# Kernel tuning notes

Hardware: AMD Instinct MI355X
Metric: run time of the kernel (lower is better)

## Reference

```python
import jax, jax.numpy as jnp
import numpy as np

N, C, H, W = 8, 80, 200, 200
PRE_NMS_THRESH = 0.05
PRE_NMS_TOP_N = 1000
NMS_THRESH = 0.6
FPN_POST_NMS_TOP_N = 100
MIN_SIZE = 0.0
TO_REMOVE = 1.0
CLASS_OFFSET = 100000.0  # > any coordinate; separates classes for class-aware NMS


def setup_inputs() -> dict:
    key = jax.random.key(0)
    k1, k2, k3, k4, k5 = jax.random.split(key, 5)
    # logits shifted so sigmoid probs sit near the 0.05 threshold (realistic sparsity)
    box_cls = jax.random.normal(k1, (N, C, H, W), jnp.float32) - 3.0
    box_regression = jax.random.uniform(k2, (N, 4, H, W), jnp.float32) * 64.0
    centerness = jax.random.normal(k3, (N, 1, H, W), jnp.float32)
    locations = jax.random.uniform(k4, (H * W, 2), jnp.float32) * 1600.0
    image_sizes = jax.random.randint(k5, (N, 2), 800, 1600, jnp.int32)  # (h, w)
    return {"locations": locations, "box_cls": box_cls,
            "box_regression": box_regression, "centerness": centerness,
            "image_sizes": image_sizes}


def _pairwise_iou(boxes):
    x1, y1, x2, y2 = boxes[:, 0], boxes[:, 1], boxes[:, 2], boxes[:, 3]
    area = (x2 - x1 + TO_REMOVE) * (y2 - y1 + TO_REMOVE)  # [K]
    iw = jnp.clip(jnp.minimum(x2[:, None], x2[None, :]) - jnp.maximum(x1[:, None], x1[None, :]) + TO_REMOVE, 0.0)
    ih = jnp.clip(jnp.minimum(y2[:, None], y2[None, :]) - jnp.maximum(y1[:, None], y1[None, :]) + TO_REMOVE, 0.0)
    inter = iw * ih
    return inter / (area[:, None] + area[None, :] - inter)


def reference(locations, box_cls, box_regression, centerness, image_sizes):
    n, c, h, w = box_cls.shape
    # [N,C,H,W] -> [N,HW,C] probs; [N,4,H,W] -> [N,HW,4]; centerness -> [N,HW]
    cls_prob = jax.nn.sigmoid(box_cls.transpose(0, 2, 3, 1).reshape(n, -1, c))
    reg = box_regression.transpose(0, 2, 3, 1).reshape(n, -1, 4)
    cent = jax.nn.sigmoid(centerness.transpose(0, 2, 3, 1).reshape(n, -1))

    def per_image(p, r, ct, hw):
        # candidate mask on raw class probs (before centerness weighting), as in source
        cand = p > PRE_NMS_THRESH                      # [HW, C]
        scores = p * ct[:, None]                       # [HW, C]
        flat = jnp.where(cand, scores, -jnp.inf).reshape(-1)
        top_s, top_i = jax.lax.top_k(flat, PRE_NMS_TOP_N)   # sorted desc
        loc_idx = top_i // c
        labels = top_i % c + 1
        valid = top_s > 0.0
        l2 = locations[loc_idx]                        # [K, 2]
        rr = r[loc_idx]                                # [K, 4]
        boxes = jnp.concatenate([l2 - rr[:, :2], l2 + rr[:, 2:]], axis=-1)
        ih = hw[0].astype(jnp.float32)
        iw = hw[1].astype(jnp.float32)
        boxes = jnp.stack([jnp.clip(boxes[:, 0], 0.0, iw - 1.0),
                           jnp.clip(boxes[:, 1], 0.0, ih - 1.0),
                           jnp.clip(boxes[:, 2], 0.0, iw - 1.0),
                           jnp.clip(boxes[:, 3], 0.0, ih - 1.0)], axis=-1)
        bw = boxes[:, 2] - boxes[:, 0] + TO_REMOVE
        bh = boxes[:, 3] - boxes[:, 1] + TO_REMOVE
        valid = valid & (bw >= MIN_SIZE) & (bh >= MIN_SIZE)
        # class-aware NMS via per-class coordinate offset
        ob = boxes + labels.astype(jnp.float32)[:, None] * CLASS_OFFSET
        iou = _pairwise_iou(ob)                        # [K, K]
        K = PRE_NMS_TOP_N
        idxs = jnp.arange(K)
        def body(supp, i):
            keep_i = valid[i] & jnp.logical_not(supp[i])
            supp = supp | (keep_i & (iou[i] > NMS_THRESH) & (idxs != i))
            return supp, keep_i
        _, keep = jax.lax.scan(body, jnp.zeros(K, dtype=bool), idxs)
        fscores = jnp.where(keep & valid, top_s, -jnp.inf)
        fs, fi = jax.lax.top_k(fscores, FPN_POST_NMS_TOP_N)
        fv = fs > 0.0
        fb = boxes[fi] * fv[:, None].astype(boxes.dtype)
        fl = jnp.where(fv, labels[fi], 0).astype(jnp.float32)
        out_s = jnp.where(fv, jnp.sqrt(jnp.where(fv, fs, 1.0)), 0.0)  # sqrt of cls*centerness
        # [K_post, 6] = x1,y1,x2,y2,score,label
        return jnp.concatenate([fb, out_s[:, None], fl[:, None]], axis=-1)

    return jax.vmap(per_image)(cls_prob, reg, cent, image_sizes)
```

## Files before the change

kernel.cpp:

```cpp
#include <hip/hip_runtime.h>
#include <math.h>

#define NIMG 8
#define NCLS 80
#define HW 40000
#define M (NCLS*HW)
#define UBINS 4096
#define CANDL 4096
#define SPILL_CAP 65536
#define BCAP 1024
#define TOPK 1000
#define OUTK 100
#define PRE_T 0.05f
#define NMS_T 0.6f
#define FLOOR_BITS 0x3E800000u
#define FLOOR_SAFE 0.2494f

__device__ unsigned int       g_scnt[NIMG][32];
__device__ unsigned int       g_ovf[NIMG];
__device__ unsigned int       g_hist[NIMG][UBINS];
__device__ unsigned short     g_xthr_b[NIMG * HW];
__device__ float              g_sct[NIMG * HW];
__device__ unsigned long long g_key[NIMG][SPILL_CAP];

__device__ __forceinline__ float sigmoid_exact(float x){
    return 1.0f / (1.0f + expf(-x));
}

__device__ __forceinline__ unsigned long long shfl_xor_u64(unsigned long long v, int j){
    int lo = __shfl_xor((int)(unsigned int)(v & 0xffffffffull), j);
    int hi = __shfl_xor((int)(unsigned int)(v >> 32), j);
    return ((unsigned long long)(unsigned int)hi << 32) | (unsigned long long)(unsigned int)lo;
}

__global__ void k0_init(const float* __restrict__ cent){
    int t = blockIdx.x * blockDim.x + threadIdx.x;
    if (t < NIMG * 32) ((unsigned int*)g_scnt)[t] = 0u;
    if (t < NIMG) g_ovf[t] = 0u;
    if (t < NIMG * UBINS) ((unsigned int*)g_hist)[t] = 0u;
    if (t < NIMG * HW){
        float pct = sigmoid_exact(cent[t]);
        g_sct[t] = pct;
        float a = FLOOR_SAFE / pct;
        float xt;
        if (a >= 1.0f) xt = 3.0e38f;
        else {
            float am = fminf(a, 0.98f);
            xt = logf(am / (1.0f - am));
        }
        unsigned xb = __float_as_uint(xt);
        unsigned hb = xb >> 16;
        if ((xb & 0x80000000u) && (xb & 0xFFFFu)) hb += 1u;
        g_xthr_b[t] = (unsigned short)hb;
    }
}

__global__ void __launch_bounds__(512, 8) k1_spill(const float* __restrict__ cls){
    const int n   = blockIdx.y;
    const int tid = threadIdx.x;
    const int e16 = blockIdx.x * 8192 + tid * 16;
    __shared__ unsigned long long skey[BCAP];
    __shared__ unsigned int lcnt, lbase;
    if (tid == 0) lcnt = 0u;
    __syncthreads();

    if (e16 < M){
        const int c   = e16 / HW;
        const int hw0 = e16 - c * HW;
        const float* pc = cls + (size_t)n * M + e16;
        const unsigned short* pt = g_xthr_b + n * HW + hw0;
        float4 xa[4];
        uint4  tb[2];
        #pragma unroll
        for (int i = 0; i < 4; ++i) xa[i] = *(const float4*)(pc + i * 4);
        tb[0] = *(const uint4*)(pt);
        tb[1] = *(const uint4*)(pt + 8);
        float th[16];
        #pragma unroll
        for (int q = 0; q < 2; ++q){
            unsigned w0 = (q?tb[1].x:tb[0].x), w1 = (q?tb[1].y:tb[0].y);
            unsigned w2 = (q?tb[1].z:tb[0].z), w3 = (q?tb[1].w:tb[0].w);
            th[q*8+0] = __uint_as_float((w0 & 0xFFFFu) << 16);
            th[q*8+1] = __uint_as_float((w0 >> 16) << 16);
            th[q*8+2] = __uint_as_float((w1 & 0xFFFFu) << 16);
            th[q*8+3] = __uint_as_float((w1 >> 16) << 16);
            th[q*8+4] = __uint_as_float((w2 & 0xFFFFu) << 16);
            th[q*8+5] = __uint_as_float((w2 >> 16) << 16);
            th[q*8+6] = __uint_as_float((w3 & 0xFFFFu) << 16);
            th[q*8+7] = __uint_as_float((w3 >> 16) << 16);
        }
        #define SPILL1(HWI, XV, THV) \
        if (XV >= THV){ \
            float p_ = sigmoid_exact(XV); \
            if (p_ > PRE_T){ \
                float s_ = p_ * g_sct[n * HW + (HWI)]; \
                unsigned long long key_ = ((unsigned long long)__float_as_uint(s_) << 32) \
                    | (unsigned long long)(0xFFFFFFFFu - (unsigned int)((HWI) * NCLS + c)); \
                atomicAdd(&g_hist[n][(int)(s_ * 4096.0f)], 1u); \
                unsigned int pp_ = atomicAdd(&lcnt, 1u); \
                if (pp_ < BCAP) skey[pp_] = key_; \
            } \
        }
        #pragma unroll
        for (int i = 0; i < 4; ++i){
            SPILL1(hw0 + i*4 + 0, xa[i].x, th[i*4+0])
            SPILL1(hw0 + i*4 + 1, xa[i].y, th[i*4+1])
            SPILL1(hw0 + i*4 + 2, xa[i].z, th[i*4+2])
            SPILL1(hw0 + i*4 + 3, xa[i].w, th[i*4+3])
        }
        #undef SPILL1
    }

    __syncthreads();
    unsigned int raw = lcnt;
    unsigned int cnt = raw < BCAP ? raw : BCAP;
    if (tid == 0){
        lbase = cnt ? atomicAdd(&g_scnt[n][0], cnt) : 0u;
        if (raw > BCAP) g_ovf[n] = 1u;
    }
    __syncthreads();
    unsigned int base = lbase;
    for (unsigned int i = tid; i < cnt; i += 512){
        unsigned int pos = base + i;
        if (pos < SPILL_CAP) g_key[n][pos] = skey[i];
    }
}

struct SelPhase {
    unsigned int hist[UBINS];
    unsigned int cs[256];
    unsigned int wtot[4];
    unsigned long long keysL[CANDL];
};
struct NmsPhase {
    float ox1[TOPK], oy1[TOPK], ox2[TOPK], oy2[TOPK], oar[TOPK];
    float bxs[TOPK][4];
    float sc[TOPK];
    int   lab[TOPK];
    int   keeplist[OUTK];
    unsigned int  Wc[16][80];
    unsigned int  ctot[80];
    unsigned int  coff[81];
    unsigned int  wcnt[16];
    unsigned short ord[1024];
    unsigned char validf[TOPK];
    unsigned char supp[TOPK];
    unsigned char keepf[1024];
};
union KU { SelPhase sel; NmsPhase nms; };

#define REGSTEP(K_, J_) { \
    unsigned long long pa = shfl_xor_u64(va, (J_)); \
    unsigned long long pb = shfl_xor_u64(vb, (J_)); \
    bool fa = ((tid & (J_)) == 0); \
    bool da = ((tid & (K_)) == 0); \
    bool db = (((tid + 1024) & (K_)) == 0); \
    va = (fa == da) ? (va > pa ? va : pa) : (va < pa ? va : pa); \
    vb = (fa == db) ? (vb > pb ? vb : pb) : (vb < pb ? vb : pb); \
}
#define REGSTEP1(K_, J_) { \
    unsigned long long pa = shfl_xor_u64(va, (J_)); \
    bool fa = ((tid & (J_)) == 0); \
    bool da = ((tid & (K_)) == 0); \
    va = (fa == da) ? (va > pa ? va : pa) : (va < pa ? va : pa); \
}

__global__ void __launch_bounds__(1024) k2_select_nms(const float* __restrict__ cls,
                                                      const float* __restrict__ loc,
                                                      const float* __restrict__ reg,
                                                      const int*   __restrict__ imsz,
                                                      float* __restrict__ out){
    const int n = blockIdx.x;
    const int tid = threadIdx.x;
    const int lane = tid & 63;
    const int wv   = tid >> 6;
    __shared__ KU u;
    __shared__ unsigned long long stop[TOPK];
    __shared__ unsigned int lcnt, s_cut, s_flag, s_nmsfb, s_cnt, s_c, s_csn, s_Cest, s_srtbad;

    for (int i = tid; i < UBINS; i += 1024) u.sel.hist[i] = g_hist[n][i];
    if (tid == 0){ s_nmsfb = 0u; s_srtbad = 0u; s_c = 0xFFFFFFFFu; s_csn = 0u;
                   s_Cest = 0u; s_cut = 0u; lcnt = 0u; }
    if (tid < TOPK) stop[tid] = 0ull;
    __syncthreads();

    unsigned int scnt_raw = g_scnt[n][0];
    unsigned int ovf_f    = g_ovf[n];
    unsigned int S = scnt_raw < SPILL_CAP ? scnt_raw : SPILL_CAP;

    if (tid < 256){
        unsigned int s = 0;
        int base = tid * 16;
        #pragma unroll
        for (int i = 0; i < 16; ++i) s += u.sel.hist[base + i];
        u.sel.cs[tid] = s;
    }
    __syncthreads();
    if (tid < 256){
        unsigned int v = u.sel.cs[tid];
        #pragma unroll
        for (int d = 1; d < 64; d <<= 1){
            unsigned int t = __shfl_down(v, d);
            if (lane + d < 64) v += t;
        }
        if (lane == 0) u.sel.wtot[wv] = v;
        u.sel.cs[tid] = v;
    }
    __syncthreads();
    if (tid < 256){
        unsigned int tail = 0;
        for (int w = wv + 1; w < 4; ++w) tail += u.sel.wtot[w];
        u.sel.cs[tid] += tail;
    }
    __syncthreads();
    if (tid < 256){
        unsigned int a = u.sel.cs[tid];
        unsigned int b = (tid == 255) ? 0u : u.sel.cs[tid + 1];
        if (a >= TOPK && b < TOPK){ s_c = (unsigned int)tid; s_csn = b; }
    }
    __syncthreads();
    if (wv == 0 && s_c != 0xFFFFFFFFu){
        unsigned int cst = s_c;
        unsigned int h = (lane < 16) ? u.sel.hist[cst * 16 + lane] : 0u;
        #pragma unroll
        for (int d = 1; d < 16; d <<= 1){
            unsigned int t = __shfl_down(h, d);
            if (lane + d < 16) h += t;
        }
        unsigned int gs  = h + s_csn;
        unsigned int gsn = __shfl_down(gs, 1);
        if (lane == 15) gsn = s_csn;
        if (lane < 16 && gs >= TOPK && gsn < TOPK){ s_cut = cst * 16 + lane; s_Cest = gs; }
    }
    __syncthreads();
    if (tid == 0){
        unsigned int c025 = u.sel.cs[64];
        s_flag = (scnt_raw > SPILL_CAP) || ovf_f || (s_c == 0xFFFFFFFFu) ||
                 (c025 < TOPK) || (s_Cest > CANDL) ? 1u : 0u;
    }
    __syncthreads();

    if (s_flag){
        for (int i = tid; i < UBINS; i += 1024) u.sel.hist[i] = 0u;
        __syncthreads();
        const float* cls_n = cls + (size_t)n * M;
        const float* sct_n = g_sct + n * HW;
        for (int e = tid; e < M; e += 1024){
            float p = sigmoid_exact(cls_n[e]);
            if (p > PRE_T){
                int c = e / HW; int hw = e - c * HW;
                float s = p * sct_n[hw];
                atomicAdd(&u.sel.hist[(int)(s * 4096.0f)], 1u);
            }
        }
        __syncthreads();
        if (tid < 256){
            unsigned int s = 0;
            int base = tid * 16;
            #pragma unroll
            for (int i = 0; i < 16; ++i) s += u.sel.hist[base + i];
            u.sel.cs[tid] = s;
        }
        __syncthreads();
        if (tid == 0){
            unsigned int acc = 0; int cut = 0; int c = 255;
            for (; c >= 0; --c){ if (acc + u.sel.cs[c] >= TOPK) break; acc += u.sel.cs[c]; }
            if (c >= 0){
                int b = c*16 + 15;
                for (;; --b){ acc += u.sel.hist[b]; if (acc >= TOPK || b == c*16) break; }
                cut = b;
            }
            while (acc > CANDL && cut < UBINS){ acc -= u.sel.hist[cut]; cut++; }
            s_cut = (unsigned int)cut;
        }
        __syncthreads();
        unsigned int cutb = s_cut;
        for (int e = tid; e < M; e += 1024){
            float p = sigmoid_exact(cls_n[e]);
            if (p > PRE_T){
                int c = e / HW; int hw = e - c * HW;
                float s = p * sct_n[hw];
                if ((int)(s * 4096.0f) >= (int)cutb){
                    unsigned int pos = atomicAdd(&lcnt, 1u);
                    if (pos < CANDL){
                        unsigned int idx = (unsigned int)(hw * NCLS + c);
                        u.sel.keysL[pos] = ((unsigned long long)__float_as_uint(s) << 32)
                                         | (unsigned long long)(0xFFFFFFFFu - idx);
                    }
                }
            }
        }
    } else {
        unsigned int cutb = s_cut;
        for (unsigned int i = tid; i < S; i += 1024){
            unsigned long long k = g_key[n][i];
            float s = __uint_as_float((unsigned int)(k >> 32));
            bool pass = ((unsigned int)(int)(s * 4096.0f)) >= cutb;
            unsigned long long mb = __ballot(pass);
            unsigned int wcnt_ = (unsigned int)__popcll(mb);
            unsigned int base = 0;
            if (lane == 0 && wcnt_) base = atomicAdd(&lcnt, wcnt_);
            base = (unsigned int)__builtin_amdgcn_readfirstlane((int)base);
            if (pass){
                unsigned int p = base + (unsigned int)__popcll(mb & ((1ull << lane) - 1ull));
                if (p < CANDL) u.sel.keysL[p] = k;
            }
        }
    }
    __syncthreads();

    int C = (int)(lcnt < CANDL ? lcnt : CANDL);
    unsigned long long kk = 0ull;
    if (C <= 1024){
        for (int i = C + tid; i < 1024; i += 1024) u.sel.keysL[i] = 0ull;
        __syncthreads();
        unsigned long long va = u.sel.keysL[tid];
        REGSTEP1(2,1)
        REGSTEP1(4,2)  REGSTEP1(4,1)
        REGSTEP1(8,4)  REGSTEP1(8,2)  REGSTEP1(8,1)
        REGSTEP1(16,8) REGSTEP1(16,4) REGSTEP1(16,2) REGSTEP1(16,1)
        REGSTEP1(32,16) REGSTEP1(32,8) REGSTEP1(32,4) REGSTEP1(32,2) REGSTEP1(32,1)
        REGSTEP1(64,32) REGSTEP1(64,16) REGSTEP1(64,8) REGSTEP1(64,4) REGSTEP1(64,2) REGSTEP1(64,1)
        for (int k = 128; k <= 1024; k <<= 1){
            u.sel.keysL[tid] = va;
            __syncthreads();
            for (int j = k >> 1; j >= 64; j >>= 1){
                if (tid < 512){
                    int i  = ((tid & ~(j - 1)) << 1) | (tid & (j - 1));
                    int p2 = i | j;
                    unsigned long long a = u.sel.keysL[i];
                    unsigned long long b = u.sel.keysL[p2];
                    bool up = ((i & k) == 0);
                    if (up ? (a < b) : (a > b)){ u.sel.keysL[i] = b; u.sel.keysL[p2] = a; }
                }
                __syncthreads();
            }
            va = u.sel.keysL[tid];
            REGSTEP1(k,32) REGSTEP1(k,16) REGSTEP1(k,8) REGSTEP1(k,4) REGSTEP1(k,2) REGSTEP1(k,1)
        }
        u.sel.keysL[tid] = va;
        __syncthreads();
        if (tid <= 1022 && u.sel.keysL[tid] < u.sel.keysL[tid + 1]) atomicOr(&s_srtbad, 1u);
        __syncthreads();
    } else if (C <= 2048){
        for (int i = C + tid; i < 2048; i += 1024) u.sel.keysL[i] = 0ull;
        __syncthreads();
        unsigned long long va = u.sel.keysL[tid];
        unsigned long long vb = u.sel.keysL[tid + 1024];
        REGSTEP(2,1)
        REGSTEP(4,2)  REGSTEP(4,1)
        REGSTEP(8,4)  REGSTEP(8,2)  REGSTEP(8,1)
        REGSTEP(16,8) REGSTEP(16,4) REGSTEP(16,2) REGSTEP(16,1)
        REGSTEP(32,16) REGSTEP(32,8) REGSTEP(32,4) REGSTEP(32,2) REGSTEP(32,1)
        REGSTEP(64,32) REGSTEP(64,16) REGSTEP(64,8) REGSTEP(64,4) REGSTEP(64,2) REGSTEP(64,1)
        for (int k = 128; k <= 2048; k <<= 1){
            if (k == 2048){
                unsigned long long mx = va > vb ? va : vb;
                unsigned long long mn = va > vb ? vb : va;
                va = mx; vb = mn;
            }
            u.sel.keysL[tid] = va; u.sel.keysL[tid + 1024] = vb;
            __syncthreads();
            for (int j = (k == 2048) ? 512 : (k >> 1); j >= 64; j >>= 1){
                int i  = ((tid & ~(j - 1)) << 1) | (tid & (j - 1));
                int p2 = i | j;
                unsigned long long a = u.sel.keysL[i];
                unsigned long long b = u.sel.keysL[p2];
                bool up = ((i & k) == 0);
                if (up ? (a < b) : (a > b)){ u.sel.keysL[i] = b; u.sel.keysL[p2] = a; }
                __syncthreads();
            }
            va = u.sel.keysL[tid]; vb = u.sel.keysL[tid + 1024];
            REGSTEP(k,32) REGSTEP(k,16) REGSTEP(k,8) REGSTEP(k,4) REGSTEP(k,2) REGSTEP(k,1)
        }
        u.sel.keysL[tid] = va; u.sel.keysL[tid + 1024] = vb;
        __syncthreads();
        bool bad = (u.sel.keysL[tid] < u.sel.keysL[tid + 1]);
        if (tid <= 1022) bad = bad || (u.sel.keysL[tid + 1024] < u.sel.keysL[tid + 1025]);
        if (bad) atomicOr(&s_srtbad, 1u);
        __syncthreads();
    } else {
        for (int i = tid; i < C; i += 1024){
            unsigned long long k = u.sel.keysL[i];
            int rank = 0;
            for (int j = 0; j < C; ++j) rank += (u.sel.keysL[j] > k) ? 1 : 0;
            if (rank < TOPK) stop[rank] = k;
        }
        __syncthreads();
        if (tid < TOPK) u.sel.keysL[tid] = stop[tid];
        __syncthreads();
    }

    if (s_srtbad){
        if (tid == 0) lcnt = 0u;
        __syncthreads();
        unsigned int cutb = s_cut;
        if (s_flag){
            const float* cls_n = cls + (size_t)n * M;
            const float* sct_n = g_sct + n * HW;
            for (int e = tid; e < M; e += 1024){
                float p = sigmoid_exact(cls_n[e]);
                if (p > PRE_T){
                    int c = e / HW; int hw = e - c * HW;
                    float s = p * sct_n[hw];
                    if ((int)(s * 4096.0f) >= (int)cutb){
                        unsigned int pos = atomicAdd(&lcnt, 1u);
                        if (pos < CANDL){
                            unsigned int idx = (unsigned int)(hw * NCLS + c);
                            u.sel.keysL[pos] = ((unsigned long long)__float_as_uint(s) << 32)
                                             | (unsigned long long)(0xFFFFFFFFu - idx);
                        }
                    }
                }
            }
        } else {
            for (unsigned int i = tid; i < S; i += 1024){
                unsigned long long k = g_key[n][i];
                float s = __uint_as_float((unsigned int)(k >> 32));
                bool pass = ((unsigned int)(int)(s * 4096.0f)) >= cutb;
                unsigned long long mb = __ballot(pass);
                unsigned int wcnt_ = (unsigned int)__popcll(mb);
                unsigned int base = 0;
                if (lane == 0 && wcnt_) base = atomicAdd(&lcnt, wcnt_);
                base = (unsigned int)__builtin_amdgcn_readfirstlane((int)base);
                if (pass){
                    unsigned int p = base + (unsigned int)__popcll(mb & ((1ull << lane) - 1ull));
                    if (p < CANDL) u.sel.keysL[p] = k;
                }
            }
        }
        __syncthreads();
        int C2 = (int)(lcnt < CANDL ? lcnt : CANDL);
        for (int i = C2 + tid; i < 2048; i += 1024) u.sel.keysL[i] = 0ull;
        __syncthreads();
        for (int k = 2; k <= 2048; k <<= 1){
            for (int j = k >> 1; j > 0; j >>= 1){
                int i  = ((tid & ~(j - 1)) << 1) | (tid & (j - 1));
                int p2 = i | j;
                unsigned long long a = u.sel.keysL[i];
                unsigned long long b = u.sel.keysL[p2];
                bool up = ((i & k) == 0);
                if (up ? (a < b) : (a > b)){ u.sel.keysL[i] = b; u.sel.keysL[p2] = a; }
                __syncthreads();
            }
        }
    }
    kk = (tid < TOPK) ? u.sel.keysL[tid] : 0ull;
    __syncthreads();

    float rx1 = 0.f, ry1 = 0.f, rx2 = -1.f, ry2 = -1.f, rar = 1.f;
    float ihh = (float)imsz[2*n + 0];
    float iww = (float)imsz[2*n + 1];

    u.nms.keepf[tid] = 0;
    { unsigned int* wz = &u.nms.Wc[0][0];
      for (int i = tid; i < 16*80; i += 1024) wz[i] = 0u; }

    if (tid < TOPK){
        unsigned int bits = (unsigned int)(kk >> 32);
        float s = __uint_as_float(bits);
        u.nms.supp[tid] = 0;
        if (s > 0.0f){
            unsigned int idx = 0xFFFFFFFFu - (unsigned int)(kk & 0xFFFFFFFFull);
            int hw = (int)(idx / NCLS);
            int c  = (int)(idx % NCLS);
            int l  = c + 1;
            float x  = loc[2*hw], y = loc[2*hw + 1];
            float r0 = reg[((size_t)n*4 + 0)*HW + hw];
            float r1 = reg[((size_t)n*4 + 1)*HW + hw];
            float r2 = reg[((size_t)n*4 + 2)*HW + hw];
            float r3 = reg[((size_t)n*4 + 3)*HW + hw];
            float x1 = fminf(fmaxf(x - r0, 0.0f), iww - 1.0f);
            float y1 = fminf(fmaxf(y - r1, 0.0f), ihh - 1.0f);
            float x2 = fminf(fmaxf(x + r2, 0.0f), iww - 1.0f);
            float y2 = fminf(fmaxf(y + r3, 0.0f), ihh - 1.0f);
            u.nms.bxs[tid][0] = x1; u.nms.bxs[tid][1] = y1;
            u.nms.bxs[tid][2] = x2; u.nms.bxs[tid][3] = y2;
            float off = (float)l * 100000.0f;
            float a1 = x1 + off, b1 = y1 + off, a2 = x2 + off, b2 = y2 + off;
            float ar = (a2 - a1 + 1.0f) * (b2 - b1 + 1.0f);
            u.nms.ox1[tid] = a1; u.nms.oy1[tid] = b1;
            u.nms.ox2[tid] = a2; u.nms.oy2[tid] = b2; u.nms.oar[tid] = ar;
            rx1 = a1; ry1 = b1; rx2 = a2; ry2 = b2; rar = ar;
            u.nms.sc[tid] = s; u.nms.lab[tid] = l; u.nms.validf[tid] = 1;
        } else {
            u.nms.validf[tid] = 0; u.nms.sc[tid] = 0.0f; u.nms.lab[tid] = 0;
            u.nms.bxs[tid][0] = u.nms.bxs[tid][1] = 0.0f;
            u.nms.bxs[tid][2] = u.nms.bxs[tid][3] = 0.0f;
            u.nms.ox1[tid] = 0.f; u.nms.oy1[tid] = 0.f;
            u.nms.ox2[tid] = -1.f; u.nms.oy2[tid] = -1.f; u.nms.oar[tid] = 1.f;
        }
    }
    __syncthreads();

    int mk = -1;
    if (tid < TOPK && u.nms.validf[tid]) mk = u.nms.lab[tid] - 1;
    if (mk >= 0) atomicAdd(&u.nms.Wc[wv][mk], 1u);
    __syncthreads();
    if (tid < NCLS){
        unsigned int acc = 0;
        for (int w = 0; w < 16; ++w){
            unsigned int v = u.nms.Wc[w][tid];
            u.nms.Wc[w][tid] = acc;
            acc += v;
        }
        u.nms.ctot[tid] = acc;
        if (acc > 64) atomicOr(&s_nmsfb, 1u);
    }
    __syncthreads();
    if (wv == 0){
        unsigned int v = u.nms.ctot[lane];
        unsigned int inc = v;
        #pragma unroll
        for (int d = 1; d < 64; d <<= 1){
            unsigned int t = __shfl_up(inc, d);
            if (lane >= d) inc += t;
        }
        u.nms.coff[lane + 1] = inc;
        if (lane == 0) u.nms.coff[0] = 0u;
        unsigned int base = __shfl(inc, 63);
        unsigned int inc2 = (lane < 16) ? u.nms.ctot[64 + lane] : 0u;
        #pragma unroll
        for (int d = 1; d < 16; d <<= 1){
            unsigned int t = __shfl_up(inc2, d);
            if (lane >= d) inc2 += t;
        }
        if (lane < 16) u.nms.coff[65 + lane] = base + inc2;
    }
    __syncthreads();

    if (!s_nmsfb){
        int below = 0;
        for (int l = 0; l < 64; ++l){
            int ok = __shfl(mk, l);
            below += (l < lane && ok == mk) ? 1 : 0;
        }
        if (mk >= 0){
            unsigned int pos = u.nms.coff[mk] + u.nms.Wc[wv][mk] + (unsigned int)below;
            u.nms.ord[pos] = (unsigned short)tid;
        }
        __syncthreads();

        for (int k = wv; k < NCLS; k += 16){
            int base = (int)u.nms.coff[k];
            int ck   = (int)u.nms.coff[k + 1] - base;
            if (ck <= 0) continue;
            int rr = (lane < ck) ? (int)u.nms.ord[base + lane] : -1;
            float bx1 = 0.f, by1 = 0.f, bx2 = -1.f, by2 = -1.f, bar = 1.f;
            if (rr >= 0){
                bx1 = u.nms.ox1[rr]; by1 = u.nms.oy1[rr];
                bx2 = u.nms.ox2[rr]; by2 = u.nms.oy2[rr]; bar = u.nms.oar[rr];
            }
            int sup = 0;
            for (int p = 0; p < ck; ++p){
                int keep_p = !__shfl(sup, p);
                if (keep_p){
                    float px1 = __shfl(bx1, p), py1 = __shfl(by1, p);
                    float px2 = __shfl(bx2, p), py2 = __shfl(by2, p);
                    float par = __shfl(bar, p);
                    if (lane > p && rr >= 0){
                        float ix1 = fmaxf(px1, bx1);
                        float iy1 = fmaxf(py1, by1);
                        float ix2 = fminf(px2, bx2);
                        float iy2 = fminf(py2, by2);
                        float iw_ = fmaxf(ix2 - ix1 + 1.0f, 0.0f);
                        float ih_ = fmaxf(iy2 - iy1 + 1.0f, 0.0f);
                        float inter = iw_ * ih_;
                        float iou = inter / (par + bar - inter);
                        if (iou > NMS_T) sup = 1;
                    }
                }
            }
            if (rr >= 0) u.nms.keepf[rr] = sup ? 0 : 1;
        }
        __syncthreads();

        int kf = (int)u.nms.keepf[tid];
        unsigned long long mb = __ballot(kf != 0);
        if (lane == 0) u.nms.wcnt[wv] = (unsigned int)__popcll(mb);
        __syncthreads();
        if (wv == 0){
            unsigned int v = (lane < 16) ? u.nms.wcnt[lane] : 0u;
            unsigned int orig = v;
            for (int d = 1; d < 16; d <<= 1){
                unsigned int t = __shfl_up(v, d);
                if (lane >= d) v += t;
            }
            if (lane < 16) u.nms.wcnt[lane] = v - orig;
            if (lane == 15) s_cnt = (v < OUTK ? v : OUTK);
        }
        __syncthreads();
        if (kf){
            unsigned int slot = u.nms.wcnt[wv] + (unsigned int)__popcll(mb & ((1ull << lane) - 1ull));
            if (slot < OUTK) u.nms.keeplist[slot] = tid;
        }
    } else {
        int cnt = 0;
        for (int i = 0; i < TOPK; ++i){
            bool keep_i = u.nms.validf[i] && !u.nms.supp[i];
            if (keep_i){
                if (tid == 0) u.nms.keeplist[cnt] = i;
                if (tid < TOPK && tid != i){
                    float ix1 = fmaxf(u.nms.ox1[i], rx1);
                    float iy1 = fmaxf(u.nms.oy1[i], ry1);
                    float ix2 = fminf(u.nms.ox2[i], rx2);
                    float iy2 = fminf(u.nms.oy2[i], ry2);
                    float iw_ = fmaxf(ix2 - ix1 + 1.0f, 0.0f);
                    float ih_ = fmaxf(iy2 - iy1 + 1.0f, 0.0f);
                    float inter = iw_ * ih_;
                    float iou = inter / (u.nms.oar[i] + rar - inter);
                    if (iou > NMS_T) u.nms.supp[tid] = 1;
                }
                cnt++;
                __syncthreads();
                if (cnt == OUTK) break;
            }
        }
        if (tid == 0) s_cnt = (unsigned int)(cnt < OUTK ? cnt : OUTK);
    }
    __syncthreads();

    int cnt = (int)s_cnt;
    if (tid < OUTK){
        float r0=0.f,r1=0.f,r2=0.f,r3=0.f,r4=0.f,r5=0.f;
        if (tid < cnt){
            int i = u.nms.keeplist[tid];
            r0 = u.nms.bxs[i][0]; r1 = u.nms.bxs[i][1];
            r2 = u.nms.bxs[i][2]; r3 = u.nms.bxs[i][3];
            r4 = sqrtf(u.nms.sc[i]); r5 = (float)u.nms.lab[i];
        }
        float* o = out + ((size_t)n*OUTK + tid)*6;
        o[0]=r0; o[1]=r1; o[2]=r2; o[3]=r3; o[4]=r4; o[5]=r5;
    }
}

extern "C" void kernel_launch(void* const* d_in, const int* in_sizes, int n_in,
                              void* d_out, int out_size, void* d_ws, size_t ws_size,
                              hipStream_t stream){
    const float* loc  = (const float*)d_in[0];
    const float* cls  = (const float*)d_in[1];
    const float* reg  = (const float*)d_in[2];
    const float* cent = (const float*)d_in[3];
    const int*   imsz = (const int*)d_in[4];
    float* out = (float*)d_out;

    hipLaunchKernelGGL(k0_init,       dim3(625),                 dim3(512),  0, stream, cent);
    hipLaunchKernelGGL(k1_spill,      dim3((M+8191)/8192, NIMG), dim3(512),  0, stream, cls);
    hipLaunchKernelGGL(k2_select_nms, dim3(NIMG),                dim3(1024), 0, stream,
                       cls, loc, reg, imsz, out);
}
```

Baseline: 238.7 us.

## Split select-and-NMS kernel into cut, parallel collect, sort and NMS kernels

The single per-image select+NMS kernel is split into four launches: a cut-bin computation, a collect step spread over 8 blocks per image that compacts spilled keys above the cut into a global candidate buffer, a register/shared bitonic sort that writes the top-1000 keys to global memory, and the NMS kernel that reads them. The aim is to parallelise the serial scan over the spill buffer, which previously ran on only 8 blocks, and to shrink the NMS kernel's shared-memory footprint. The cost is three extra kernel launches and global-memory round trips, plus a global atomic counter for candidate compaction. The fallback path (flag set) now re-runs the full-scan path inside the NMS kernel.

After: 240.1 us. Within noise of the previous version (+0.6%).

```diff
diff --git a/kernel.cpp b/kernel.cpp
--- a/kernel.cpp
+++ b/kernel.cpp
@@ -22,6 +22,11 @@
 __device__ unsigned short     g_xthr_b[NIMG * HW];
 __device__ float              g_sct[NIMG * HW];
 __device__ unsigned long long g_key[NIMG][SPILL_CAP];
+__device__ unsigned int       g_cut[NIMG];
+__device__ unsigned int       g_flag[NIMG];
+__device__ unsigned int       g_ccnt[NIMG][32];
+__device__ unsigned long long g_cand[NIMG][CANDL];
+__device__ unsigned long long g_top[NIMG][TOPK];
 
 __device__ __forceinline__ float sigmoid_exact(float x){
     return 1.0f / (1.0f + expf(-x));
@@ -36,6 +41,7 @@
 __global__ void k0_init(const float* __restrict__ cent){
     int t = blockIdx.x * blockDim.x + threadIdx.x;
     if (t < NIMG * 32) ((unsigned int*)g_scnt)[t] = 0u;
+    if (t < NIMG * 32) ((unsigned int*)g_ccnt)[t] = 0u;
     if (t < NIMG) g_ovf[t] = 0u;
     if (t < NIMG * UBINS) ((unsigned int*)g_hist)[t] = 0u;
     if (t < NIMG * HW){
@@ -126,10 +132,212 @@
     }
 }
 
+
+__global__ void __launch_bounds__(1024) k2a_cut(){
+    const int n = blockIdx.x;
+    const int tid = threadIdx.x;
+    const int lane = tid & 63;
+    const int wv   = tid >> 6;
+    __shared__ unsigned int hist[UBINS];
+    __shared__ unsigned int cs[256];
+    __shared__ unsigned int wtot[4];
+    __shared__ unsigned int s_c, s_csn, s_cut, s_Cest;
+
+    for (int i = tid; i < UBINS; i += 1024) hist[i] = g_hist[n][i];
+    if (tid == 0){ s_c = 0xFFFFFFFFu; s_csn = 0u; s_cut = 0u; s_Cest = 0u; }
+    __syncthreads();
+
+    unsigned int scnt_raw = g_scnt[n][0];
+    unsigned int ovf_f    = g_ovf[n];
+
+    if (tid < 256){
+        unsigned int s = 0;
+        int base = tid * 16;
+        #pragma unroll
+        for (int i = 0; i < 16; ++i) s += hist[base + i];
+        cs[tid] = s;
+    }
+    __syncthreads();
+    if (tid < 256){
+        unsigned int v = cs[tid];
+        #pragma unroll
+        for (int d = 1; d < 64; d <<= 1){
+            unsigned int t = __shfl_down(v, d);
+            if (lane + d < 64) v += t;
+        }
+        if (lane == 0) wtot[wv] = v;
+        cs[tid] = v;
+    }
+    __syncthreads();
+    if (tid < 256){
+        unsigned int tail = 0;
+        for (int w = wv + 1; w < 4; ++w) tail += wtot[w];
+        cs[tid] += tail;
+    }
+    __syncthreads();
+    if (tid < 256){
+        unsigned int a = cs[tid];
+        unsigned int b = (tid == 255) ? 0u : cs[tid + 1];
+        if (a >= TOPK && b < TOPK){ s_c = (unsigned int)tid; s_csn = b; }
+    }
+    __syncthreads();
+    if (wv == 0 && s_c != 0xFFFFFFFFu){
+        unsigned int cst = s_c;
+        unsigned int h = (lane < 16) ? hist[cst * 16 + lane] : 0u;
+        #pragma unroll
+        for (int d = 1; d < 16; d <<= 1){
+            unsigned int t = __shfl_down(h, d);
+            if (lane + d < 16) h += t;
+        }
+        unsigned int gs  = h + s_csn;
+        unsigned int gsn = __shfl_down(gs, 1);
+        if (lane == 15) gsn = s_csn;
+        if (lane < 16 && gs >= TOPK && gsn < TOPK){ s_cut = cst * 16 + lane; s_Cest = gs; }
+    }
+    __syncthreads();
+    if (tid == 0){
+        unsigned int c025 = cs[64];
+        unsigned int fl = (scnt_raw > SPILL_CAP) || ovf_f || (s_c == 0xFFFFFFFFu) ||
+                          (c025 < TOPK) || (s_Cest > 2048u) ? 1u : 0u;
+        g_cut[n]  = s_cut;
+        g_flag[n] = fl;
+    }
+}
+
+__global__ void __launch_bounds__(1024) k2b_collect(){
+    const int slice = blockIdx.x;
+    const int n     = blockIdx.y;
+    const int tid   = threadIdx.x;
+    const int lane  = tid & 63;
+    if (g_flag[n]) return;
+    unsigned int scnt_raw = g_scnt[n][0];
+    unsigned int S = scnt_raw < SPILL_CAP ? scnt_raw : SPILL_CAP;
+    unsigned int chunk = (S + 7) / 8;
+    unsigned int lo = slice * chunk;
+    unsigned int hi = lo + chunk; if (hi > S) hi = S;
+    unsigned int cutb = g_cut[n];
+    for (unsigned int i = lo + tid; i < hi; i += 1024){
+        unsigned long long k = g_key[n][i];
+        float s = __uint_as_float((unsigned int)(k >> 32));
+        bool pass = ((unsigned int)(int)(s * 4096.0f)) >= cutb;
+        unsigned long long mb = __ballot(pass);
+        unsigned int wcnt_ = (unsigned int)__popcll(mb);
+        unsigned int base = 0;
+        if (lane == 0 && wcnt_) base = atomicAdd(&g_ccnt[n][0], wcnt_);
+        base = (unsigned int)__builtin_amdgcn_readfirstlane((int)base);
+        if (pass){
+            unsigned int p = base + (unsigned int)__popcll(mb & ((1ull << lane) - 1ull));
+            if (p < CANDL) g_cand[n][p] = k;
+        }
+    }
+}
+
+#define REGSTEP(K_, J_) { \
+    unsigned long long pa = shfl_xor_u64(va, (J_)); \
+    unsigned long long pb = shfl_xor_u64(vb, (J_)); \
+    bool fa = ((tid & (J_)) == 0); \
+    bool da = ((tid & (K_)) == 0); \
+    bool db = (((tid + 1024) & (K_)) == 0); \
+    va = (fa == da) ? (va > pa ? va : pa) : (va < pa ? va : pa); \
+    vb = (fa == db) ? (vb > pb ? vb : pb) : (vb < pb ? vb : pb); \
+}
+#define REGSTEP1(K_, J_) { \
+    unsigned long long pa = shfl_xor_u64(va, (J_)); \
+    bool fa = ((tid & (J_)) == 0); \
+    bool da = ((tid & (K_)) == 0); \
+    va = (fa == da) ? (va > pa ? va : pa) : (va < pa ? va : pa); \
+}
+
+__global__ void __launch_bounds__(1024) k2c_sort(){
+    const int n = blockIdx.x;
+    const int tid = threadIdx.x;
+    __shared__ unsigned long long keysL[2048];
+    __shared__ unsigned int s_srtbad;
+    if (g_flag[n]) return;
+    if (tid == 0) s_srtbad = 0u;
+    int C = (int)g_ccnt[n][0];
+    if (C > 2048){ if (tid == 0) atomicOr(&g_flag[n], 2u); return; }
+    for (int i = tid; i < C; i += 1024) if (i < C) keysL[i] = g_cand[n][i];
+    __syncthreads();
+
+    if (C <= 1024){
+        for (int i = C + tid; i < 1024; i += 1024) keysL[i] = 0ull;
+        __syncthreads();
+        unsigned long long va = keysL[tid & 1023];
+        if (tid < 1024){
+            REGSTEP1(2,1)
+            REGSTEP1(4,2)  REGSTEP1(4,1)
+            REGSTEP1(8,4)  REGSTEP1(8,2)  REGSTEP1(8,1)
+            REGSTEP1(16,8) REGSTEP1(16,4) REGSTEP1(16,2) REGSTEP1(16,1)
+            REGSTEP1(32,16) REGSTEP1(32,8) REGSTEP1(32,4) REGSTEP1(32,2) REGSTEP1(32,1)
+            REGSTEP1(64,32) REGSTEP1(64,16) REGSTEP1(64,8) REGSTEP1(64,4) REGSTEP1(64,2) REGSTEP1(64,1)
+        }
+        for (int k = 128; k <= 1024; k <<= 1){
+            keysL[tid] = va;
+            __syncthreads();
+            for (int j = k >> 1; j >= 64; j >>= 1){
+                if (tid < 512){
+                    int i  = ((tid & ~(j - 1)) << 1) | (tid & (j - 1));
+                    int p2 = i | j;
+                    unsigned long long a = keysL[i];
+                    unsigned long long b = keysL[p2];
+                    bool up = ((i & k) == 0);
+                    if (up ? (a < b) : (a > b)){ keysL[i] = b; keysL[p2] = a; }
+                }
+                __syncthreads();
+            }
+            va = keysL[tid];
+            REGSTEP1(k,32) REGSTEP1(k,16) REGSTEP1(k,8) REGSTEP1(k,4) REGSTEP1(k,2) REGSTEP1(k,1)
+        }
+        keysL[tid] = va;
+        __syncthreads();
+        if (tid <= 1022 && keysL[tid] < keysL[tid + 1]) atomicOr(&s_srtbad, 1u);
+        __syncthreads();
+    } else {
+        for (int i = C + tid; i < 2048; i += 1024) keysL[i] = 0ull;
+        __syncthreads();
+        unsigned long long va = keysL[tid];
+        unsigned long long vb = keysL[tid + 1024];
+        REGSTEP(2,1)
+        REGSTEP(4,2)  REGSTEP(4,1)
+        REGSTEP(8,4)  REGSTEP(8,2)  REGSTEP(8,1)
+        REGSTEP(16,8) REGSTEP(16,4) REGSTEP(16,2) REGSTEP(16,1)
+        REGSTEP(32,16) REGSTEP(32,8) REGSTEP(32,4) REGSTEP(32,2) REGSTEP(32,1)
+        REGSTEP(64,32) REGSTEP(64,16) REGSTEP(64,8) REGSTEP(64,4) REGSTEP(64,2) REGSTEP(64,1)
+        for (int k = 128; k <= 2048; k <<= 1){
+            if (k == 2048){
+                unsigned long long mx = va > vb ? va : vb;
+                unsigned long long mn = va > vb ? vb : va;
+                va = mx; vb = mn;
+            }
+            keysL[tid] = va; keysL[tid + 1024] = vb;
+            __syncthreads();
+            for (int j = (k == 2048) ? 512 : (k >> 1); j >= 64; j >>= 1){
+                int i  = ((tid & ~(j - 1)) << 1) | (tid & (j - 1));
+                int p2 = i | j;
+                unsigned long long a = keysL[i];
+                unsigned long long b = keysL[p2];
+                bool up = ((i & k) == 0);
+                if (up ? (a < b) : (a > b)){ keysL[i] = b; keysL[p2] = a; }
+                __syncthreads();
+            }
+            va = keysL[tid]; vb = keysL[tid + 1024];
+            REGSTEP(k,32) REGSTEP(k,16) REGSTEP(k,8) REGSTEP(k,4) REGSTEP(k,2) REGSTEP(k,1)
+        }
+        keysL[tid] = va; keysL[tid + 1024] = vb;
+        __syncthreads();
+        bool bad = (keysL[tid] < keysL[tid + 1]);
+        if (tid <= 1022) bad = bad || (keysL[tid + 1024] < keysL[tid + 1025]);
+        if (bad) atomicOr(&s_srtbad, 1u);
+        __syncthreads();
+    }
+    if (s_srtbad){ if (tid == 0) atomicOr(&g_flag[n], 2u); return; }
+    if (tid < TOPK) g_top[n][tid] = keysL[tid];
+}
+
 struct SelPhase {
     unsigned int hist[UBINS];
     unsigned int cs[256];
-    unsigned int wtot[4];
     unsigned long long keysL[CANDL];
 };
 struct NmsPhase {
@@ -149,99 +357,28 @@
 };
 union KU { SelPhase sel; NmsPhase nms; };
 
-#define REGSTEP(K_, J_) { \
-    unsigned long long pa = shfl_xor_u64(va, (J_)); \
-    unsigned long long pb = shfl_xor_u64(vb, (J_)); \
-    bool fa = ((tid & (J_)) == 0); \
-    bool da = ((tid & (K_)) == 0); \
-    bool db = (((tid + 1024) & (K_)) == 0); \
-    va = (fa == da) ? (va > pa ? va : pa) : (va < pa ? va : pa); \
-    vb = (fa == db) ? (vb > pb ? vb : pb) : (vb < pb ? vb : pb); \
-}
-#define REGSTEP1(K_, J_) { \
-    unsigned long long pa = shfl_xor_u64(va, (J_)); \
-    bool fa = ((tid & (J_)) == 0); \
-    bool da = ((tid & (K_)) == 0); \
-    va = (fa == da) ? (va > pa ? va : pa) : (va < pa ? va : pa); \
-}
-
-__global__ void __launch_bounds__(1024) k2_select_nms(const float* __restrict__ cls,
-                                                      const float* __restrict__ loc,
-                                                      const float* __restrict__ reg,
-                                                      const int*   __restrict__ imsz,
-                                                      float* __restrict__ out){
+__global__ void __launch_bounds__(1024) k2d_nms(const float* __restrict__ cls,
+                                                const float* __restrict__ loc,
+                                                const float* __restrict__ reg,
+                                                const int*   __restrict__ imsz,
+                                                float* __restrict__ out){
     const int n = blockIdx.x;
     const int tid = threadIdx.x;
     const int lane = tid & 63;
     const int wv   = tid >> 6;
     __shared__ KU u;
     __shared__ unsigned long long stop[TOPK];
-    __shared__ unsigned int lcnt, s_cut, s_flag, s_nmsfb, s_cnt, s_c, s_csn, s_Cest, s_srtbad;
-
-    for (int i = tid; i < UBINS; i += 1024) u.sel.hist[i] = g_hist[n][i];
-    if (tid == 0){ s_nmsfb = 0u; s_srtbad = 0u; s_c = 0xFFFFFFFFu; s_csn = 0u;
-                   s_Cest = 0u; s_cut = 0u; lcnt = 0u; }
-    if (tid < TOPK) stop[tid] = 0ull;
-    __syncthreads();
-
-    unsigned int scnt_raw = g_scnt[n][0];
-    unsigned int ovf_f    = g_ovf[n];
-    unsigned int S = scnt_raw < SPILL_CAP ? scnt_raw : SPILL_CAP;
-
-    if (tid < 256){
-        unsigned int s = 0;
-        int base = tid * 16;
-        #pragma unroll
-        for (int i = 0; i < 16; ++i) s += u.sel.hist[base + i];
-        u.sel.cs[tid] = s;
-    }
-    __syncthreads();
-    if (tid < 256){
-        unsigned int v = u.sel.cs[tid];
-        #pragma unroll
-        for (int d = 1; d < 64; d <<= 1){
-            unsigned int t = __shfl_down(v, d);
-            if (lane + d < 64) v += t;
-        }
-        if (lane == 0) u.sel.wtot[wv] = v;
-        u.sel.cs[tid] = v;
-    }
-    __syncthreads();
-    if (tid < 256){
-        unsigned int tail = 0;
-        for (int w = wv + 1; w < 4; ++w) tail += u.sel.wtot[w];
-        u.sel.cs[tid] += tail;
-    }
-    __syncthreads();
-    if (tid < 256){
-        unsigned int a = u.sel.cs[tid];
-        unsigned int b = (tid == 255) ? 0u : u.sel.cs[tid + 1];
-        if (a >= TOPK && b < TOPK){ s_c = (unsigned int)tid; s_csn = b; }
-    }
-    __syncthreads();
-    if (wv == 0 && s_c != 0xFFFFFFFFu){
-        unsigned int cst = s_c;
-        unsigned int h = (lane < 16) ? u.sel.hist[cst * 16 + lane] : 0u;
-        #pragma unroll
-        for (int d = 1; d < 16; d <<= 1){
-            unsigned int t = __shfl_down(h, d);
-            if (lane + d < 16) h += t;
-        }
-        unsigned int gs  = h + s_csn;
-        unsigned int gsn = __shfl_down(gs, 1);
-        if (lane == 15) gsn = s_csn;
-        if (lane < 16 && gs >= TOPK && gsn < TOPK){ s_cut = cst * 16 + lane; s_Cest = gs; }
-    }
-    __syncthreads();
-    if (tid == 0){
-        unsigned int c025 = u.sel.cs[64];
-        s_flag = (scnt_raw > SPILL_CAP) || ovf_f || (s_c == 0xFFFFFFFFu) ||
-                 (c025 < TOPK) || (s_Cest > CANDL) ? 1u : 0u;
-    }
-    __syncthreads();
-
-    if (s_flag){
+    __shared__ unsigned int lcnt, s_cut, s_nmsfb, s_cnt;
+
+    unsigned long long kk = 0ull;
+    unsigned int flag = g_flag[n];
+
+    if (!flag){
+        kk = (tid < TOPK) ? g_top[n][tid] : 0ull;
+    } else {
         for (int i = tid; i < UBINS; i += 1024) u.sel.hist[i] = 0u;
+        if (tid == 0) lcnt = 0u;
+        if (tid < TOPK) stop[tid] = 0ull;
         __syncthreads();
         const float* cls_n = cls + (size_t)n * M;
         const float* sct_n = g_sct + n * HW;
@@ -290,164 +427,37 @@
                 }
             }
         }
-    } else {
-        unsigned int cutb = s_cut;
-        for (unsigned int i = tid; i < S; i += 1024){
-            unsigned long long k = g_key[n][i];
-            float s = __uint_as_float((unsigned int)(k >> 32));
-            bool pass = ((unsigned int)(int)(s * 4096.0f)) >= cutb;
-            unsigned long long mb = __ballot(pass);
-            unsigned int wcnt_ = (unsigned int)__popcll(mb);
-            unsigned int base = 0;
-            if (lane == 0 && wcnt_) base = atomicAdd(&lcnt, wcnt_);
-            base = (unsigned int)__builtin_amdgcn_readfirstlane((int)base);
-            if (pass){
-                unsigned int p = base + (unsigned int)__popcll(mb & ((1ull << lane) - 1ull));
-                if (p < CANDL) u.sel.keysL[p] = k;
-            }
-        }
-    }
-    __syncthreads();
-
-    int C = (int)(lcnt < CANDL ? lcnt : CANDL);
-    unsigned long long kk = 0ull;
-    if (C <= 1024){
-        for (int i = C + tid; i < 1024; i += 1024) u.sel.keysL[i] = 0ull;
-        __syncthreads();
-        unsigned long long va = u.sel.keysL[tid];
-        REGSTEP1(2,1)
-        REGSTEP1(4,2)  REGSTEP1(4,1)
-        REGSTEP1(8,4)  REGSTEP1(8,2)  REGSTEP1(8,1)
-        REGSTEP1(16,8) REGSTEP1(16,4) REGSTEP1(16,2) REGSTEP1(16,1)
-        REGSTEP1(32,16) REGSTEP1(32,8) REGSTEP1(32,4) REGSTEP1(32,2) REGSTEP1(32,1)
-        REGSTEP1(64,32) REGSTEP1(64,16) REGSTEP1(64,8) REGSTEP1(64,4) REGSTEP1(64,2) REGSTEP1(64,1)
-        for (int k = 128; k <= 1024; k <<= 1){
-            u.sel.keysL[tid] = va;
+        __syncthreads();
+        int C = (int)(lcnt < CANDL ? lcnt : CANDL);
+        if (C <= 2048){
+            for (int i = C + tid; i < 2048; i += 1024) u.sel.keysL[i] = 0ull;
             __syncthreads();
-            for (int j = k >> 1; j >= 64; j >>= 1){
-                if (tid < 512){
+            for (int k = 2; k <= 2048; k <<= 1){
+                for (int j = k >> 1; j > 0; j >>= 1){
                     int i  = ((tid & ~(j - 1)) << 1) | (tid & (j - 1));
                     int p2 = i | j;
                     unsigned long long a = u.sel.keysL[i];
                     unsigned long long b = u.sel.keysL[p2];
                     bool up = ((i & k) == 0);
                     if (up ? (a < b) : (a > b)){ u.sel.keysL[i] = b; u.sel.keysL[p2] = a; }
+                    __syncthreads();
                 }
-                __syncthreads();
-            }
-            va = u.sel.keysL[tid];
-            REGSTEP1(k,32) REGSTEP1(k,16) REGSTEP1(k,8) REGSTEP1(k,4) REGSTEP1(k,2) REGSTEP1(k,1)
-        }
-        u.sel.keysL[tid] = va;
-        __syncthreads();
-        if (tid <= 1022 && u.sel.keysL[tid] < u.sel.keysL[tid + 1]) atomicOr(&s_srtbad, 1u);
-        __syncthreads();
-    } else if (C <= 2048){
-        for (int i = C + tid; i < 2048; i += 1024) u.sel.keysL[i] = 0ull;
-        __syncthreads();
-        unsigned long long va = u.sel.keysL[tid];
-        unsigned long long vb = u.sel.keysL[tid + 1024];
-        REGSTEP(2,1)
-        REGSTEP(4,2)  REGSTEP(4,1)
-        REGSTEP(8,4)  REGSTEP(8,2)  REGSTEP(8,1)
-        REGSTEP(16,8) REGSTEP(16,4) REGSTEP(16,2) REGSTEP(16,1)
-        REGSTEP(32,16) REGSTEP(32,8) REGSTEP(32,4) REGSTEP(32,2) REGSTEP(32,1)
-        REGSTEP(64,32) REGSTEP(64,16) REGSTEP(64,8) REGSTEP(64,4) REGSTEP(64,2) REGSTEP(64,1)
-        for (int k = 128; k <= 2048; k <<= 1){
-            if (k == 2048){
-                unsigned long long mx = va > vb ? va : vb;
-                unsigned long long mn = va > vb ? vb : va;
-                va = mx; vb = mn;
-            }
-            u.sel.keysL[tid] = va; u.sel.keysL[tid + 1024] = vb;
+            }
+            kk = (tid < TOPK) ? u.sel.keysL[tid] : 0ull;
+        } else {
+            for (int i = tid; i < C; i += 1024){
+                unsigned long long k = u.sel.keysL[i];
+                int rank = 0;
+                for (int j = 0; j < C; ++j) rank += (u.sel.keysL[j] > k) ? 1 : 0;
+                if (rank < TOPK) stop[rank] = k;
+            }
             __syncthreads();
-            for (int j = (k == 2048) ? 512 : (k >> 1); j >= 64; j >>= 1){
-                int i  = ((tid & ~(j - 1)) << 1) | (tid & (j - 1));
-                int p2 = i | j;
-                unsigned long long a = u.sel.keysL[i];
-                unsigned long long b = u.sel.keysL[p2];
-                bool up = ((i & k) == 0);
-                if (up ? (a < b) : (a > b)){ u.sel.keysL[i] = b; u.sel.keysL[p2] = a; }
-                __syncthreads();
-            }
-            va = u.sel.keysL[tid]; vb = u.sel.keysL[tid + 1024];
-            REGSTEP(k,32) REGSTEP(k,16) REGSTEP(k,8) REGSTEP(k,4) REGSTEP(k,2) REGSTEP(k,1)
-        }
-        u.sel.keysL[tid] = va; u.sel.keysL[tid + 1024] = vb;
-        __syncthreads();
-        bool bad = (u.sel.keysL[tid] < u.sel.keysL[tid + 1]);
-        if (tid <= 1022) bad = bad || (u.sel.keysL[tid + 1024] < u.sel.keysL[tid + 1025]);
-        if (bad) atomicOr(&s_srtbad, 1u);
-        __syncthreads();
-    } else {
-        for (int i = tid; i < C; i += 1024){
-            unsigned long long k = u.sel.keysL[i];
-            int rank = 0;
-            for (int j = 0; j < C; ++j) rank += (u.sel.keysL[j] > k) ? 1 : 0;
-            if (rank < TOPK) stop[rank] = k;
-        }
-        __syncthreads();
-        if (tid < TOPK) u.sel.keysL[tid] = stop[tid];
-        __syncthreads();
-    }
-
-    if (s_srtbad){
-        if (tid == 0) lcnt = 0u;
-        __syncthreads();
-        unsigned int cutb = s_cut;
-        if (s_flag){
-            const float* cls_n = cls + (size_t)n * M;
-            const float* sct_n = g_sct + n * HW;
-            for (int e = tid; e < M; e += 1024){
-                float p = sigmoid_exact(cls_n[e]);
-                if (p > PRE_T){
-                    int c = e / HW; int hw = e - c * HW;
-                    float s = p * sct_n[hw];
-                    if ((int)(s * 4096.0f) >= (int)cutb){
-                        unsigned int pos = atomicAdd(&lcnt, 1u);
-                        if (pos < CANDL){
-                            unsigned int idx = (unsigned int)(hw * NCLS + c);
-                            u.sel.keysL[pos] = ((unsigned long long)__float_as_uint(s) << 32)
-                                             | (unsigned long long)(0xFFFFFFFFu - idx);
-                        }
-                    }
-                }
-            }
-        } else {
-            for (unsigned int i = tid; i < S; i += 1024){
-                unsigned long long k = g_key[n][i];
-                float s = __uint_as_float((unsigned int)(k >> 32));
-                bool pass = ((unsigned int)(int)(s * 4096.0f)) >= cutb;
-                unsigned long long mb = __ballot(pass);
-                unsigned int wcnt_ = (unsigned int)__popcll(mb);
-                unsigned int base = 0;
-                if (lane == 0 && wcnt_) base = atomicAdd(&lcnt, wcnt_);
-                base = (unsigned int)__builtin_amdgcn_readfirstlane((int)base);
-                if (pass){
-                    unsigned int p = base + (unsigned int)__popcll(mb & ((1ull << lane) - 1ull));
-                    if (p < CANDL) u.sel.keysL[p] = k;
-                }
-            }
-        }
-        __syncthreads();
-        int C2 = (int)(lcnt < CANDL ? lcnt : CANDL);
-        for (int i = C2 + tid; i < 2048; i += 1024) u.sel.keysL[i] = 0ull;
-        __syncthreads();
-        for (int k = 2; k <= 2048; k <<= 1){
-            for (int j = k >> 1; j > 0; j >>= 1){
-                int i  = ((tid & ~(j - 1)) << 1) | (tid & (j - 1));
-                int p2 = i | j;
-                unsigned long long a = u.sel.keysL[i];
-                unsigned long long b = u.sel.keysL[p2];
-                bool up = ((i & k) == 0);
-                if (up ? (a < b) : (a > b)){ u.sel.keysL[i] = b; u.sel.keysL[p2] = a; }
-                __syncthreads();
-            }
-        }
-    }
-    kk = (tid < TOPK) ? u.sel.keysL[tid] : 0ull;
-    __syncthreads();
-
+            kk = (tid < TOPK) ? stop[tid] : 0ull;
+        }
+    }
+    __syncthreads();
+
+    if (tid == 0) s_nmsfb = 0u;
     float rx1 = 0.f, ry1 = 0.f, rx2 = -1.f, ry2 = -1.f, rar = 1.f;
     float ihh = (float)imsz[2*n + 0];
     float iww = (float)imsz[2*n + 1];
@@ -644,8 +654,11 @@
     const int*   imsz = (const int*)d_in[4];
     float* out = (float*)d_out;
 
-    hipLaunchKernelGGL(k0_init,       dim3(625),                 dim3(512),  0, stream, cent);
-    hipLaunchKernelGGL(k1_spill,      dim3((M+8191)/8192, NIMG), dim3(512),  0, stream, cls);
-    hipLaunchKernelGGL(k2_select_nms, dim3(NIMG),                dim3(1024), 0, stream,
+    hipLaunchKernelGGL(k0_init,     dim3(625),                 dim3(512),  0, stream, cent);
+    hipLaunchKernelGGL(k1_spill,    dim3((M+8191)/8192, NIMG), dim3(512),  0, stream, cls);
+    hipLaunchKernelGGL(k2a_cut,     dim3(NIMG),                dim3(1024), 0, stream);
+    hipLaunchKernelGGL(k2b_collect, dim3(8, NIMG),             dim3(1024), 0, stream);
+    hipLaunchKernelGGL(k2c_sort,    dim3(NIMG),                dim3(1024), 0, stream);
+    hipLaunchKernelGGL(k2d_nms,     dim3(NIMG),                dim3(1024), 0, stream,
                        cls, loc, reg, imsz, out);
 }
```
